# Performance work log

Hardware: AMD Instinct MI355X
Metric: run time of the kernel (lower is better)

The kernel has to match this reference:

```python
import jax, jax.numpy as jnp
import numpy as np

B, C, H, W = 8, 16, 128, 128
P = H * W            # pixel_number = 16384
KN = 16              # kernel_number_per_pixel
CK = C * 9           # in_channel * kernel_size = 144


def setup_inputs() -> dict:
    key = jax.random.key(0)
    k1, k2, k3 = jax.random.split(key, 3)
    x = jax.random.normal(k1, (B, C, H, W), dtype=jnp.float32)
    weights = jax.random.normal(k2, (P, KN, CK), dtype=jnp.float32)
    hash_idx = jax.random.randint(k3, (P, CK), 0, C * H * W, dtype=jnp.int64)
    return {"x": x, "weights": weights, "hash_idx": hash_idx}


def reference(x, weights, hash_idx):
    b, c, h, w = x.shape
    img_size = c * h * w
    flat = x.reshape(-1)  # [B*C*H*W]
    # per-batch offset of the per-pixel hash table (torch fallback branch)
    idx = hash_idx[None, :, :] + (jnp.arange(b, dtype=hash_idx.dtype) * img_size)[:, None, None]  # [B,P,CK]
    patches = flat[idx]  # [B, P, CK] hash-indexed gather (im2col)
    # weights [P,KN,CK] @ patches [P,CK,B] -> [P,KN,B]; transpose(0,2) -> [B,KN,P]
    return jnp.einsum('pkc,bpc->bkp', weights, patches)
```

## Files before the change

### kernel.cpp

```cpp
#include <hip/hip_runtime.h>
#include <hip/hip_bf16.h>

#define P_TOTAL 16384
#define KN      16
#define CK      144
#define BATCH   8
#define IMG     262144
#define RWH     176

typedef __attribute__((ext_vector_type(8))) short bf16x8;
typedef __attribute__((ext_vector_type(4))) float f32x4;

__device__ __forceinline__ short f2bf(float f) {
    __hip_bfloat16 h = __float2bfloat16(f);
    return *reinterpret_cast<short*>(&h);
}

__global__ __launch_bounds__(256) void transpose_x_bf16(
    const float* __restrict__ x, float4* __restrict__ xt)
{
    const int i = blockIdx.x * 256 + threadIdx.x;
    union { short h[8]; float4 f4; } u;
#pragma unroll
    for (int b = 0; b < BATCH; ++b)
        u.h[b] = f2bf(x[(size_t)b * IMG + i]);
    xt[i] = u.f4;
}

__global__ __launch_bounds__(256) void abc2d_mfma(
    const float4* __restrict__ xt,
    const float*  __restrict__ w,
    const int*    __restrict__ hidx,
    float* __restrict__ out)
{
    __shared__ short patchT[4 * 8 * RWH];

    const int t    = threadIdx.x;
    const int wv   = t >> 6;
    const int lane = t & 63;
    const int bid  = blockIdx.x;
    const int p = (bid & 7) * (P_TOTAL / 8) + (bid >> 3) * 4 + wv;

    short* pT = patchT + wv * 8 * RWH;

    const int* hp = hidx + p * CK;
    const int c0 = lane, c1 = lane + 64;
    const int id0 = hp[c0];
    const int id1 = hp[c1];
    int id2 = 0;
    if (lane < 16) id2 = hp[lane + 128];
    union { short h[8]; float4 f4; } u0, u1, u2;
    u0.f4 = xt[id0];
    u1.f4 = xt[id1];
    if (lane < 16) u2.f4 = xt[id2];
#pragma unroll
    for (int b = 0; b < BATCH; ++b) pT[b * RWH + c0] = u0.h[b];
#pragma unroll
    for (int b = 0; b < BATCH; ++b) pT[b * RWH + c1] = u1.h[b];
    if (lane < 16) {
#pragma unroll
        for (int b = 0; b < BATCH; ++b) pT[b * RWH + lane + 128] = u2.h[b];
    }
    reinterpret_cast<int*>(pT)[(lane >> 3) * 88 + 72 + (lane & 7)] = 0;

    const int n    = lane & 15;
    const int q    = lane >> 4;
    const int arow = n & 7;
    const short* aptr = pT + arow * RWH;
    const float* wp   = w + (size_t)p * (KN * CK) + (size_t)n * CK;

    f32x4 acc = {0.f, 0.f, 0.f, 0.f};
#pragma unroll
    for (int s = 0; s < 5; ++s) {
        const int c = 32 * s + 8 * q;
        bf16x8 a = *reinterpret_cast<const bf16x8*>(aptr + c);
        bf16x8 b = {0, 0, 0, 0, 0, 0, 0, 0};
        if (c < CK) {
            const float4 f0 = *reinterpret_cast<const float4*>(wp + c);
            const float4 f1 = *reinterpret_cast<const float4*>(wp + c + 4);
            b[0] = f2bf(f0.x); b[1] = f2bf(f0.y); b[2] = f2bf(f0.z); b[3] = f2bf(f0.w);
            b[4] = f2bf(f1.x); b[5] = f2bf(f1.y); b[6] = f2bf(f1.z); b[7] = f2bf(f1.w);
        }
        acc = __builtin_amdgcn_mfma_f32_16x16x32_bf16(a, b, acc, 0, 0, 0);
    }

    if (lane < 32) {
#pragma unroll
        for (int i = 0; i < 4; ++i) {
            const int b = q * 4 + i;
            out[(size_t)b * (KN * P_TOTAL) + (size_t)n * P_TOTAL + p] = acc[i];
        }
    }
}

__global__ __launch_bounds__(256) void abc2d_fallback(
    const float* __restrict__ x, const float* __restrict__ w,
    const int* __restrict__ hidx, float* __restrict__ out)
{
    __shared__ float patch[CK * 12];
    const int bid = blockIdx.x;
    const int p   = (bid & 7) * (P_TOTAL / 8) + (bid >> 3);
    const int t   = threadIdx.x;
    const int* hp = hidx + p * CK;
    for (int j = t; j < CK * BATCH; j += 256) {
        const int c = j >> 3, b = j & 7;
        patch[c * 12 + b] = x[(size_t)hp[c] + (size_t)b * IMG];
    }
    __syncthreads();
    const int k = t >> 4, cs = t & 15;
    const float* wp = w + (size_t)p * (KN * CK) + (size_t)k * CK;
    float acc[BATCH];
#pragma unroll
    for (int b = 0; b < BATCH; ++b) acc[b] = 0.f;
#pragma unroll
    for (int i = 0; i < 9; ++i) {
        const int c = cs + 16 * i;
        const float wv = wp[c];
        const float* pr = &patch[c * 12];
#pragma unroll
        for (int b = 0; b < BATCH; ++b) acc[b] += wv * pr[b];
    }
#pragma unroll
    for (int b = 0; b < BATCH; ++b) {
        float v = acc[b];
        v += __shfl_xor(v, 1); v += __shfl_xor(v, 2);
        v += __shfl_xor(v, 4); v += __shfl_xor(v, 8);
        acc[b] = v;
    }
    if (cs == 0)
#pragma unroll
        for (int b = 0; b < BATCH; ++b)
            out[(size_t)b * (KN * P_TOTAL) + (size_t)k * P_TOTAL + p] = acc[b];
}

extern "C" void kernel_launch(void* const* d_in, const int* in_sizes, int n_in,
                              void* d_out, int out_size, void* d_ws, size_t ws_size,
                              hipStream_t stream) {
    const float* x    = (const float*)d_in[0];
    const float* wts  = (const float*)d_in[1];
    const int*   hidx = (const int*)d_in[2];
    float* out = (float*)d_out;

    const size_t xt_bytes = (size_t)IMG * BATCH * sizeof(short);
    if (ws_size >= xt_bytes) {
        float4* xt = (float4*)d_ws;
        transpose_x_bf16<<<IMG / 256, 256, 0, stream>>>(x, xt);
        abc2d_mfma<<<P_TOTAL / 4, 256, 0, stream>>>(xt, wts, hidx, out);
    } else {
        abc2d_fallback<<<P_TOTAL, 256, 0, stream>>>(x, wts, hidx, out);
    }
}
```

Before: 241.4 us.

## Split fused gather+MFMA kernel into separate gather and GEMM kernels via workspace

Splits the single kernel into two. The first gathers hash-indexed bf16 patches into a global workspace buffer, and the second loads those patches from global memory and runs the MFMA GEMM with the weights. This removes the shared-memory staging and lets the random gathers and the weight streaming each run in their own kernel. In exchange it adds an extra launch and a round trip of about 42 MB through global memory, and needs a larger workspace, or the code drops to the slow fallback.

```diff
diff --git a/kernel.cpp b/kernel.cpp
--- a/kernel.cpp
+++ b/kernel.cpp
@@ -6,7 +6,7 @@
 #define CK      144
 #define BATCH   8
 #define IMG     262144
-#define RWH     176
+#define PATCH_H 160
 
 typedef __attribute__((ext_vector_type(8))) short bf16x8;
 typedef __attribute__((ext_vector_type(4))) float f32x4;
@@ -27,53 +27,61 @@
     xt[i] = u.f4;
 }
 
-__global__ __launch_bounds__(256) void abc2d_mfma(
+__global__ __launch_bounds__(256) void gather_patches(
     const float4* __restrict__ xt,
-    const float*  __restrict__ w,
     const int*    __restrict__ hidx,
-    float* __restrict__ out)
+    unsigned short* __restrict__ patches)
 {
-    __shared__ short patchT[4 * 8 * RWH];
-
     const int t    = threadIdx.x;
     const int wv   = t >> 6;
     const int lane = t & 63;
     const int bid  = blockIdx.x;
-    const int p = (bid & 7) * (P_TOTAL / 8) + (bid >> 3) * 4 + wv;
-
-    short* pT = patchT + wv * 8 * RWH;
+    const int p    = (bid & 7) * (P_TOTAL / 8) + (bid >> 3) * 4 + wv;
 
     const int* hp = hidx + p * CK;
-    const int c0 = lane, c1 = lane + 64;
-    const int id0 = hp[c0];
-    const int id1 = hp[c1];
-    int id2 = 0;
-    if (lane < 16) id2 = hp[lane + 128];
-    union { short h[8]; float4 f4; } u0, u1, u2;
-    u0.f4 = xt[id0];
-    u1.f4 = xt[id1];
-    if (lane < 16) u2.f4 = xt[id2];
+    unsigned short* pp = patches + (size_t)p * BATCH * PATCH_H;
+
+    union { unsigned short h[8]; float4 f4; } u0, u1, u2;
+    u0.f4 = xt[hp[lane]];
+    u1.f4 = xt[hp[lane + 64]];
+    const bool tail = lane < (CK - 128);
+    if (tail) u2.f4 = xt[hp[lane + 128]];
+
 #pragma unroll
-    for (int b = 0; b < BATCH; ++b) pT[b * RWH + c0] = u0.h[b];
+    for (int b = 0; b < BATCH; ++b) pp[b * PATCH_H + lane]       = u0.h[b];
 #pragma unroll
-    for (int b = 0; b < BATCH; ++b) pT[b * RWH + c1] = u1.h[b];
-    if (lane < 16) {
+    for (int b = 0; b < BATCH; ++b) pp[b * PATCH_H + lane + 64]  = u1.h[b];
+    if (tail) {
 #pragma unroll
-        for (int b = 0; b < BATCH; ++b) pT[b * RWH + lane + 128] = u2.h[b];
+        for (int b = 0; b < BATCH; ++b) pp[b * PATCH_H + lane + 128] = u2.h[b];
+    } else if (lane < 32) {
+#pragma unroll
+        for (int b = 0; b < BATCH; ++b) pp[b * PATCH_H + lane + 128] = 0;
     }
-    reinterpret_cast<int*>(pT)[(lane >> 3) * 88 + 72 + (lane & 7)] = 0;
+}
+
+__global__ __launch_bounds__(256) void gemm_mfma(
+    const unsigned short* __restrict__ patches,
+    const float* __restrict__ w,
+    float* __restrict__ out)
+{
+    const int t    = threadIdx.x;
+    const int wv   = t >> 6;
+    const int lane = t & 63;
+    const int bid  = blockIdx.x;
+    const int p    = (bid & 7) * (P_TOTAL / 8) + (bid >> 3) * 4 + wv;
 
     const int n    = lane & 15;
     const int q    = lane >> 4;
     const int arow = n & 7;
-    const short* aptr = pT + arow * RWH;
-    const float* wp   = w + (size_t)p * (KN * CK) + (size_t)n * CK;
+    const unsigned short* ap = patches + (size_t)p * BATCH * PATCH_H + (size_t)arow * PATCH_H;
+    const float* wp = w + (size_t)p * (KN * CK) + (size_t)n * CK;
 
     f32x4 acc = {0.f, 0.f, 0.f, 0.f};
 #pragma unroll
     for (int s = 0; s < 5; ++s) {
         const int c = 32 * s + 8 * q;
-        bf16x8 a = *reinterpret_cast<const bf16x8*>(aptr + c);
+        bf16x8 a = *reinterpret_cast<const bf16x8*>(ap + c);
         bf16x8 b = {0, 0, 0, 0, 0, 0, 0, 0};
         if (c < CK) {
             const float4 f0 = *reinterpret_cast<const float4*>(wp + c);
@@ -141,11 +149,16 @@
     const int*   hidx = (const int*)d_in[2];
     float* out = (float*)d_out;
 
-    const size_t xt_bytes = (size_t)IMG * BATCH * sizeof(short);
-    if (ws_size >= xt_bytes) {
+    const size_t xt_bytes    = (size_t)IMG * BATCH * sizeof(short);
+    const size_t patch_bytes = (size_t)P_TOTAL * BATCH * PATCH_H * sizeof(short);
+    const size_t patch_off   = 8u << 20;
+
+    if (ws_size >= patch_off + patch_bytes) {
         float4* xt = (float4*)d_ws;
+        unsigned short* patches = (unsigned short*)((char*)d_ws + patch_off);
         transpose_x_bf16<<<IMG / 256, 256, 0, stream>>>(x, xt);
-        abc2d_mfma<<<P_TOTAL / 4, 256, 0, stream>>>(xt, wts, hidx, out);
+        gather_patches<<<P_TOTAL / 4, 256, 0, stream>>>(xt, hidx, patches);
+        gemm_mfma<<<P_TOTAL / 4, 256, 0, stream>>>(patches, wts, out);
     } else {
         abc2d_fallback<<<P_TOTAL, 256, 0, stream>>>(x, wts, hidx, out);
     }
```

Measured after the change: 256.9 us. 6.4% more time.
